# Kernel tuning notes

Measured on AMD Instinct MI355X. Metric: run time of the kernel, lower is better.

Reference implementation:

```python
import jax, jax.numpy as jnp
import numpy as np

N_NODES = 50000
N_EDGES = 800000
N_GRAPHS = 256
NEG_SLOPE = 0.2  # PyG GATConv default leaky_relu slope


def gat_conv(x, edge_index, W, a_src, a_dst, bias, concat):
    # x: [N, F_in], edge_index: [2, E] (row=source, col=dest), W: [F_in, H*C]
    N = x.shape[0]
    H, C = a_src.shape
    h = (x @ W).reshape(N, H, C)                       # [N, H, C]
    s_src = (h * a_src).sum(-1)                        # [N, H]
    s_dst = (h * a_dst).sum(-1)                        # [N, H]
    src, dst = edge_index[0], edge_index[1]
    alpha = jax.nn.leaky_relu(s_src[src] + s_dst[dst], NEG_SLOPE)  # [E, H]
    # softmax over edges grouped by destination node
    m = jax.ops.segment_max(alpha, dst, num_segments=N)
    alpha = jnp.exp(alpha - m[dst])
    denom = jax.ops.segment_sum(alpha, dst, num_segments=N)
    alpha = alpha / (denom[dst] + 1e-16)
    out = jax.ops.segment_sum(h[src] * alpha[:, :, None], dst, num_segments=N)  # [N, H, C]
    out = out.reshape(N, H * C) if concat else out.mean(axis=1)
    return out + bias


def setup_inputs() -> dict:
    key = jax.random.key(0)
    ks = jax.random.split(key, 12)
    x = jax.random.normal(ks[0], (N_NODES, 27), dtype=jnp.float32)
    edge_index = jax.random.randint(ks[1], (2, N_EDGES), 0, N_NODES, dtype=jnp.int64 if jax.config.jax_enable_x64 else jnp.int32)
    batch = (jnp.arange(N_NODES) * N_GRAPHS) // N_NODES  # sorted, every graph non-empty
    g = lambda k, shape, fan_in: jax.random.normal(k, shape, dtype=jnp.float32) * (1.0 / np.sqrt(fan_in))
    return {
        "x": x, "edge_index": edge_index, "batch": batch,
        "W1": g(ks[2], (27, 64), 27), "a_src1": g(ks[3], (4, 16), 16), "a_dst1": g(ks[4], (4, 16), 16), "b1": jnp.zeros((64,), jnp.float32),
        "W2": g(ks[5], (64, 256), 64), "a_src2": g(ks[6], (1, 256), 256), "a_dst2": g(ks[7], (1, 256), 256), "b2": jnp.zeros((256,), jnp.float32),
        "Wl1": g(ks[8], (256, 512), 256), "bl1": jnp.zeros((512,), jnp.float32),
        "Wl2": g(ks[9], (512, 1024), 512), "bl2": jnp.zeros((1024,), jnp.float32),
        "Wl3": g(ks[10], (1024, 4), 1024), "bl3": jnp.zeros((4,), jnp.float32),
    }


def reference(x, edge_index, batch, W1, a_src1, a_dst1, b1, W2, a_src2, a_dst2, b2, Wl1, bl1, Wl2, bl2, Wl3, bl3):
    N = x.shape[0]
    # add self loops (PyG GATConv default)
    loops = jnp.arange(N, dtype=edge_index.dtype)
    ei = jnp.concatenate([edge_index, jnp.stack([loops, loops])], axis=1)
    h = jax.nn.elu(gat_conv(x, ei, W1, a_src1, a_dst1, b1, concat=True))    # [N, 64]
    h = jax.nn.elu(gat_conv(h, ei, W2, a_src2, a_dst2, b2, concat=False))   # [N, 256]
    # global max pool per graph
    pooled = jax.ops.segment_max(h, batch, num_segments=N_GRAPHS)           # [G, 256]
    z = jax.nn.relu(pooled @ Wl1 + bl1)
    z = jax.nn.relu(z @ Wl2 + bl2)
    return z @ Wl3 + bl3                                                    # [G, 4] logits (CrossEntropyLoss branch)
```

## Files before the change

### kernel.cpp

```cpp
#include <hip/hip_runtime.h>
#include <hip/hip_fp16.h>
#include <math.h>

#define NEG_SLOPE 0.2f
#define SCANB 256
#define CAP 6144

__device__ __forceinline__ float leaky(float x) { return x >= 0.f ? x : NEG_SLOPE * x; }
__device__ __forceinline__ float elu(float x) { return x > 0.f ? x : expm1f(x); }

__device__ __forceinline__ unsigned encf(float f) {
    unsigned u = __float_as_uint(f);
    return (u & 0x80000000u) ? ~u : (u | 0x80000000u);
}

struct Half4 { __half2 a, b; };

typedef _Float16 half8 __attribute__((ext_vector_type(8)));
typedef float floatx4 __attribute__((ext_vector_type(4)));


__global__ __launch_bounds__(1024) void k_passA(const int* __restrict__ src,
                                                const int* __restrict__ dst, int E, int nbuck,
                                                int2* __restrict__ tmp, int* __restrict__ bcursor) {
    __shared__ int cnt[256];
    __shared__ int base[256];
    int t = threadIdx.x;
    if (t < 256) cnt[t] = 0;
    __syncthreads();
    int e0 = blockIdx.x * 4096;
    int s[4], d[4], r[4];
    bool v[4];
#pragma unroll
    for (int i = 0; i < 4; ++i) {
        int e = e0 + i * 1024 + t;
        v[i] = e < E;
        if (v[i]) {
            s[i] = src[e];
            d[i] = dst[e];
            r[i] = atomicAdd(&cnt[d[i] >> 8], 1);
        }
    }
    __syncthreads();
    if (t < nbuck) {
        int c = cnt[t];
        base[t] = c ? atomicAdd(&bcursor[t], c) : 0;
    }
    __syncthreads();
#pragma unroll
    for (int i = 0; i < 4; ++i) {
        if (v[i]) {
            int b = d[i] >> 8;
            int pos = base[b] + r[i];
            if (pos < CAP) tmp[(size_t)b * CAP + pos] = make_int2(s[i], d[i]);
        }
    }
}

__global__ __launch_bounds__(256) void k_B1s(const int2* __restrict__ tmp,
                                             const int* __restrict__ bcursor,
                                             int* __restrict__ offs, int* __restrict__ bsum,
                                             int N) {
    __shared__ int cnt[256];
    __shared__ int sm[256];
    int b = blockIdx.x, t = threadIdx.x;
    cnt[t] = 0;
    __syncthreads();
    int n = bcursor[b];
    if (n > CAP) n = CAP;
    for (int j = t; j < n; j += 256)
        atomicAdd(&cnt[tmp[(size_t)b * CAP + j].y & 255], 1);
    __syncthreads();
    int node = b * 256 + t;
    int v = (node < N) ? cnt[t] + 1 : 0;
    sm[t] = v;
    __syncthreads();
    for (int off = 1; off < 256; off <<= 1) {
        int u = (t >= off) ? sm[t - off] : 0;
        __syncthreads();
        sm[t] += u;
        __syncthreads();
    }
    if (node < N) offs[node] = sm[t] - v;
    if (t == 255) bsum[b] = sm[255];
}

__global__ void k_scan2(int* __restrict__ bsum, int nb) {
    __shared__ int sm[SCANB];
    int v = (threadIdx.x < nb) ? bsum[threadIdx.x] : 0;
    sm[threadIdx.x] = v;
    __syncthreads();
    for (int off = 1; off < SCANB; off <<= 1) {
        int t = (threadIdx.x >= off) ? sm[threadIdx.x - off] : 0;
        __syncthreads();
        sm[threadIdx.x] += t;
        __syncthreads();
    }
    if (threadIdx.x < nb) bsum[threadIdx.x] = sm[threadIdx.x] - v;
}

__global__ void k_scan3(int* __restrict__ offs, const int* __restrict__ bsum,
                        int* __restrict__ csr, int N, int EN) {
    int i = blockIdx.x * SCANB + threadIdx.x;
    if (i < N) {
        int v = offs[i] + bsum[blockIdx.x];
        offs[i] = v;
        csr[v] = i;
        if (i == N - 1) offs[N] = EN;
    }
}

__global__ __launch_bounds__(256) void k_B2(const int2* __restrict__ tmp,
                                            const int* __restrict__ bcursor,
                                            const int* __restrict__ offs,
                                            int* __restrict__ csr, int N) {
    __shared__ int cnt[256];
    int b = blockIdx.x, t = threadIdx.x;
    cnt[t] = 0;
    __syncthreads();
    int n = bcursor[b];
    if (n > CAP) n = CAP;
    for (int j = t; j < n; j += 256) {
        int2 sd = tmp[(size_t)b * CAP + j];
        int r = atomicAdd(&cnt[sd.y & 255], 1);
        csr[offs[sd.y] + 1 + r] = sd.x;
    }
}

__global__ void k_prep(const float* __restrict__ W2, __half* __restrict__ W2t,
                       const float* __restrict__ Wl1, __half* __restrict__ Wl1t,
                       const float* __restrict__ Wl2, __half* __restrict__ Wl2t,
                       const float* __restrict__ a_src2, const float* __restrict__ a_dst2,
                       float* __restrict__ ws2, float* __restrict__ wd2) {
    int i = blockIdx.x * blockDim.x + threadIdx.x;
    if (i < 16384) {
        int k = i >> 8, n = i & 255;
        W2t[(size_t)n * 64 + k] = __float2half(W2[i]);
    } else if (i < 16384 + 131072) {
        int j = i - 16384;
        int k = j >> 9, n = j & 511;
        Wl1t[(size_t)n * 256 + k] = __float2half(Wl1[j]);
    } else if (i < 16384 + 131072 + 524288) {
        int j = i - 16384 - 131072;
        int k = j >> 10, n = j & 1023;
        Wl2t[(size_t)n * 512 + k] = __float2half(Wl2[j]);
    } else if (i < 16384 + 131072 + 524288 + 128) {
        int j = i - 16384 - 131072 - 524288;
        int k = j & 63;
        const float* av = (j < 64) ? a_src2 : a_dst2;
        float acc = 0.f;
        for (int c = 0; c < 256; ++c) acc += W2[k * 256 + c] * av[c];
        if (j < 64) ws2[k] = acc; else wd2[k] = acc;
    }
}


__global__ void k_h1(const float* __restrict__ x, const float* __restrict__ W1,
                     const float* __restrict__ a_src, const float* __restrict__ a_dst,
                     __half* __restrict__ h1h, float* __restrict__ ssrc, float* __restrict__ sdst,
                     int N) {
    __shared__ float sW[27 * 64];
    for (int i = threadIdx.x; i < 27 * 64; i += blockDim.x) sW[i] = W1[i];
    __syncthreads();
    int wave = threadIdx.x >> 6;
    int lane = threadIdx.x & 63;
    int n = blockIdx.x * 4 + wave;
    if (n >= N) return;
    const float* xr = x + (size_t)n * 27;
    float acc = 0.f;
#pragma unroll
    for (int k = 0; k < 27; ++k) acc += xr[k] * sW[k * 64 + lane];
    h1h[(size_t)n * 64 + lane] = __float2half(acc);
    int hd = lane >> 4, c = lane & 15;
    float vs = acc * a_src[hd * 16 + c];
    float vd = acc * a_dst[hd * 16 + c];
#pragma unroll
    for (int off = 8; off >= 1; off >>= 1) {
        vs += __shfl_xor(vs, off);
        vd += __shfl_xor(vd, off);
    }
    if (c == 0) {
        ssrc[n * 4 + hd] = vs;
        sdst[n * 4 + hd] = vd;
    }
}

__global__ void k_msd1(const int* __restrict__ csr, const int* __restrict__ offs,
                       const float* __restrict__ ssrc, const float* __restrict__ sdst,
                       __half* __restrict__ e4h, float* __restrict__ dinv4, int N) {
    int i = blockIdx.x * blockDim.x + threadIdx.x;
    if (i >= N * 4) return;
    int n = i >> 2, hd = i & 3;
    int start = offs[n];
    int dg = offs[n + 1] - start;
    float sd = sdst[(size_t)n * 4 + hd];
    float den = 0.f;
    for (int j = 0; j < dg; ++j) {
        int s = csr[start + j];
        float e = expf(leaky(ssrc[(size_t)s * 4 + hd] + sd));
        den += e;
        e4h[(size_t)(start + j) * 4 + hd] = __float2half(e);
    }
    dinv4[(size_t)n * 4 + hd] = 1.f / (den + 1e-16f);
}

__global__ __launch_bounds__(64) void k_agg1(
        const int* __restrict__ csr, const int* __restrict__ offs,
        const __half* __restrict__ e4h, const float* __restrict__ dinv4,
        const __half* __restrict__ h1h, const float* __restrict__ bias,
        const float* __restrict__ ws2, const float* __restrict__ wd2,
        __half* __restrict__ out, float* __restrict__ ssrc2, float* __restrict__ sdst2, int N) {
    int d = blockIdx.x;
    int lane = threadIdx.x;
    int start = offs[d];
    int dg = offs[d + 1] - start;
    int hd = lane >> 4;
    float acc = 0.f;
#pragma unroll 4
    for (int j = 0; j < dg; ++j) {
        int s = csr[start + j];
        float w = __half2float(e4h[(size_t)(start + j) * 4 + hd]);
        acc += __half2float(h1h[(size_t)s * 64 + lane]) * w;
    }
    acc *= dinv4[(size_t)d * 4 + hd];
    float av = elu(acc + bias[lane]);
    out[(size_t)d * 64 + lane] = __float2half(av);
    float vs = av * ws2[lane];
    float vd = av * wd2[lane];
#pragma unroll
    for (int off = 32; off >= 1; off >>= 1) {
        vs += __shfl_xor(vs, off);
        vd += __shfl_xor(vd, off);
    }
    if (lane == 0) { ssrc2[d] = vs; sdst2[d] = vd; }
}


__global__ void k_msd2(const int* __restrict__ csr, const int* __restrict__ offs,
                       const float* __restrict__ ssrc, const float* __restrict__ sdst,
                       __half* __restrict__ e1h, float* __restrict__ dinv1, int N) {
    int n = blockIdx.x * blockDim.x + threadIdx.x;
    if (n >= N) return;
    int start = offs[n];
    int dg = offs[n + 1] - start;
    float sd = sdst[n];
    float den = 0.f;
#pragma unroll 2
    for (int j = 0; j < dg; ++j) {
        float e = expf(leaky(ssrc[csr[start + j]] + sd));
        den += e;
        e1h[start + j] = __float2half(e);
    }
    dinv1[n] = 1.f / (den + 1e-16f);
}

__global__ __launch_bounds__(64) void k_agg2(
        const int* __restrict__ csr, const int* __restrict__ offs,
        const __half* __restrict__ e1h, const float* __restrict__ dinv1,
        const __half* __restrict__ act1h, __half* __restrict__ aggh, int N) {
    int d = blockIdx.x;
    int lane = threadIdx.x;
    int start = offs[d];
    int dg = offs[d + 1] - start;
    float acc = 0.f;
#pragma unroll 4
    for (int j = 0; j < dg; ++j) {
        int s = csr[start + j];
        float w = __half2float(e1h[start + j]);
        acc += __half2float(act1h[(size_t)s * 64 + lane]) * w;
    }
    acc *= dinv1[d];
    aggh[(size_t)d * 64 + lane] = __float2half(acc);
}

__global__ void k_h2b(const __half* __restrict__ aggh, const __half* __restrict__ W2t,
                      const float* __restrict__ b2, const int* __restrict__ batch,
                      unsigned* __restrict__ pooledU, int N) {
    int t = threadIdx.x;
    int wv = t >> 6, lane = t & 63;
    int lr = lane & 15, lg = lane >> 4;
    int n0 = blockIdx.x * 16;

    half8 a0 = {0, 0, 0, 0, 0, 0, 0, 0};
    half8 a1 = {0, 0, 0, 0, 0, 0, 0, 0};
    int nodeA = n0 + lr;
    if (nodeA < N) {
        a0 = *(const half8*)(aggh + (size_t)nodeA * 64 + lg * 8);
        a1 = *(const half8*)(aggh + (size_t)nodeA * 64 + 32 + lg * 8);
    }
    int gFirst = batch[n0];
    int gLast  = batch[min(n0 + 15, N - 1)];
    bool uni = (gFirst == gLast);
#pragma unroll
    for (int c = 0; c < 4; ++c) {
        int col = wv * 64 + c * 16 + lr;
        half8 b0 = *(const half8*)(W2t + (size_t)col * 64 + lg * 8);
        half8 b1 = *(const half8*)(W2t + (size_t)col * 64 + 32 + lg * 8);
        floatx4 acc = {0.f, 0.f, 0.f, 0.f};
        acc = __builtin_amdgcn_mfma_f32_16x16x32_f16(a0, b0, acc, 0, 0, 0);
        acc = __builtin_amdgcn_mfma_f32_16x16x32_f16(a1, b1, acc, 0, 0, 0);
        float bv = b2[col];
        float v0 = elu(acc[0] + bv);
        float v1 = elu(acc[1] + bv);
        float v2 = elu(acc[2] + bv);
        float v3 = elu(acc[3] + bv);
        if (uni) {
            float vm = fmaxf(fmaxf(v0, v1), fmaxf(v2, v3));
            vm = fmaxf(vm, __shfl_xor(vm, 16));
            vm = fmaxf(vm, __shfl_xor(vm, 32));
            if (lg == 0) atomicMax(&pooledU[gFirst * 256 + col], encf(vm));
        } else {
            float vr[4] = {v0, v1, v2, v3};
#pragma unroll
            for (int r = 0; r < 4; ++r) {
                int node = n0 + lg * 4 + r;
                if (node < N) atomicMax(&pooledU[batch[node] * 256 + col], encf(vr[r]));
            }
        }
    }
}

__global__ void k_dec(const unsigned* __restrict__ pooledU, __half* __restrict__ pooledh) {
    int i = blockIdx.x * 256 + threadIdx.x;
    unsigned u = pooledU[i];
    u = (u & 0x80000000u) ? (u & 0x7FFFFFFFu) : ~u;
    pooledh[i] = __float2half(__uint_as_float(u));
}


__global__ void k_gemm(const __half* __restrict__ A, const __half* __restrict__ Wt,
                       const float* __restrict__ bias, __half* __restrict__ C,
                       int M, int N, int K, int relu) {
    int t = threadIdx.x;
    int wv = t >> 6, lane = t & 63;
    int lr = lane & 15, lg = lane >> 4;
    int bx = blockIdx.x, by = blockIdx.y;
    int arow = by * 64 + wv * 16 + lr;
    floatx4 acc[4] = {{0.f,0.f,0.f,0.f},{0.f,0.f,0.f,0.f},{0.f,0.f,0.f,0.f},{0.f,0.f,0.f,0.f}};
    for (int k0 = 0; k0 < K; k0 += 32) {
        half8 a = *(const half8*)(A + (size_t)arow * K + k0 + lg * 8);
#pragma unroll
        for (int c = 0; c < 4; ++c) {
            int col = bx * 64 + c * 16 + lr;
            half8 b = *(const half8*)(Wt + (size_t)col * K + k0 + lg * 8);
            acc[c] = __builtin_amdgcn_mfma_f32_16x16x32_f16(a, b, acc[c], 0, 0, 0);
        }
    }
#pragma unroll
    for (int c = 0; c < 4; ++c) {
        int col = bx * 64 + c * 16 + lr;
        float bv = bias[col];
#pragma unroll
        for (int r = 0; r < 4; ++r) {
            int row = by * 64 + wv * 16 + lg * 4 + r;
            float v = acc[c][r] + bv;
            if (relu) v = fmaxf(v, 0.f);
            C[(size_t)row * N + col] = __float2half(v);
        }
    }
}

__global__ void k_mlp3(const __half* __restrict__ z2, const float* __restrict__ Wl3,
                       const float* __restrict__ bl3, float* __restrict__ out, int G) {
    __shared__ float sT[16];
    int g = blockIdx.x, t = threadIdx.x;
    int wave = t >> 6, lane = t & 63;
    float p[4] = {0.f, 0.f, 0.f, 0.f};
#pragma unroll
    for (int kk = 0; kk < 4; ++kk) {
        int k = t + kk * 256;
        float z = __half2float(z2[(size_t)g * 1024 + k]);
        float4 w = ((const float4*)Wl3)[k];
        p[0] += z * w.x; p[1] += z * w.y; p[2] += z * w.z; p[3] += z * w.w;
    }
#pragma unroll
    for (int c = 0; c < 4; ++c) {
#pragma unroll
        for (int off = 32; off >= 1; off >>= 1) p[c] += __shfl_xor(p[c], off);
        if (lane == 0) sT[wave * 4 + c] = p[c];
    }
    __syncthreads();
    if (t < 4) {
        float v = bl3[t] + sT[t] + sT[4 + t] + sT[8 + t] + sT[12 + t];
        out[(size_t)g * 4 + t] = v;
    }
}

extern "C" void kernel_launch(void* const* d_in, const int* in_sizes, int n_in,
                              void* d_out, int out_size, void* d_ws, size_t ws_size,
                              hipStream_t stream) {
    const float* x      = (const float*)d_in[0];
    const int*   ei     = (const int*)d_in[1];
    const int*   batch  = (const int*)d_in[2];
    const float* W1     = (const float*)d_in[3];
    const float* a_src1 = (const float*)d_in[4];
    const float* a_dst1 = (const float*)d_in[5];
    const float* b1     = (const float*)d_in[6];
    const float* W2     = (const float*)d_in[7];
    const float* a_src2 = (const float*)d_in[8];
    const float* a_dst2 = (const float*)d_in[9];
    const float* b2     = (const float*)d_in[10];
    const float* Wl1    = (const float*)d_in[11];
    const float* bl1    = (const float*)d_in[12];
    const float* Wl2    = (const float*)d_in[13];
    const float* bl2    = (const float*)d_in[14];
    const float* Wl3    = (const float*)d_in[15];
    const float* bl3    = (const float*)d_in[16];

    const int N = in_sizes[0] / 27;
    const int E = in_sizes[1] / 2;
    const int G = out_size / 4;
    const int EN = E + N;
    const int nbuck = (N + 255) >> 8;

    const int* srcA = ei;
    const int* dstA = ei + E;

    char* wp = (char*)d_ws;
    auto take = [&](size_t bytes) { char* p = wp; wp += (bytes + 15) & ~(size_t)15; return p; };

    int2* tmp     = (int2*)take((size_t)256 * CAP * 8);
    int* bcursor  = (int*)take(256 * 4);
    int* offs     = (int*)take((size_t)(N + 1) * 4);
    int* bsum     = (int*)take((size_t)SCANB * 4);
    int* csr      = (int*)take((size_t)EN * 4);

    float* ssrc1  = (float*)take((size_t)N * 4 * 4);
    float* sdst1  = (float*)take((size_t)N * 4 * 4);
    float* ssrc2  = (float*)take((size_t)N * 4);
    float* sdst2  = (float*)take((size_t)N * 4);
    float* dinv4  = (float*)take((size_t)N * 4 * 4);
    float* dinv1  = (float*)take((size_t)N * 4);
    float* ws2    = (float*)take(64 * 4);
    float* wd2    = (float*)take(64 * 4);
    unsigned* pooledU = (unsigned*)take((size_t)G * 256 * 4);

    __half* h1h   = (__half*)take((size_t)N * 64 * 2);
    __half* act1h = (__half*)take((size_t)N * 64 * 2);
    __half* aggh  = (__half*)take((size_t)N * 64 * 2);
    __half* e4h   = (__half*)take((size_t)EN * 4 * 2);
    __half* e1h   = (__half*)take((size_t)EN * 2);
    __half* W2t   = (__half*)take((size_t)64 * 256 * 2);
    __half* Wl1t  = (__half*)take((size_t)512 * 256 * 2);
    __half* Wl2t  = (__half*)take((size_t)1024 * 512 * 2);
    __half* pooledh = (__half*)take((size_t)G * 256 * 2);
    __half* z1h   = (__half*)take((size_t)G * 512 * 2);
    __half* z2h   = (__half*)take((size_t)G * 1024 * 2);

    const int nb = (N + SCANB - 1) / SCANB;

    {
        int tot = 16384 + 131072 + 524288 + 128;
        k_prep<<<(tot + 255) / 256, 256, 0, stream>>>(W2, W2t, Wl1, Wl1t, Wl2, Wl2t,
                                                      a_src2, a_dst2, ws2, wd2);
    }

    hipMemsetAsync(bcursor, 0, 256 * 4, stream);
    hipMemsetAsync(pooledU, 0, (size_t)G * 256 * 4, stream);
    k_passA<<<(E + 4095) / 4096, 1024, 0, stream>>>(srcA, dstA, E, nbuck, tmp, bcursor);
    k_B1s<<<nbuck, 256, 0, stream>>>(tmp, bcursor, offs, bsum, N);
    k_scan2<<<1, SCANB, 0, stream>>>(bsum, nb);
    k_scan3<<<nb, SCANB, 0, stream>>>(offs, bsum, csr, N, EN);
    k_B2<<<nbuck, 256, 0, stream>>>(tmp, bcursor, offs, csr, N);

    k_h1<<<(N + 3) / 4, 256, 0, stream>>>(x, W1, a_src1, a_dst1, h1h, ssrc1, sdst1, N);
    k_msd1<<<(N * 4 + 255) / 256, 256, 0, stream>>>(csr, offs, ssrc1, sdst1, e4h, dinv4, N);
    k_agg1<<<N, 64, 0, stream>>>(csr, offs, e4h, dinv4, h1h, b1, ws2, wd2,
                                 act1h, ssrc2, sdst2, N);

    k_msd2<<<(N + 255) / 256, 256, 0, stream>>>(csr, offs, ssrc2, sdst2, e1h, dinv1, N);
    k_agg2<<<N, 64, 0, stream>>>(csr, offs, e1h, dinv1, act1h, aggh, N);
    k_h2b<<<(N + 15) / 16, 256, 0, stream>>>(aggh, W2t, b2, batch, pooledU, N);

    k_dec<<<G, 256, 0, stream>>>(pooledU, pooledh);
    k_gemm<<<dim3(512 / 64, 256 / 64), 256, 0, stream>>>(pooledh, Wl1t, bl1, z1h, 256, 512, 256, 1);
    k_gemm<<<dim3(1024 / 64, 256 / 64), 256, 0, stream>>>(z1h, Wl2t, bl2, z2h, 256, 1024, 512, 1);
    k_mlp3<<<G, 256, 0, stream>>>(z2h, Wl3, bl3, (float*)d_out, G);
}
```

Before: 207.7 us.

## Fuse preprocessing, CSR build and MLP tail kernels to cut launch count

Merges the bucket pass with the weight prep into one launch, and folds the three CSR scan kernels into a single kernel that uses a decoupled lookback over per-block aggregates. The pooled-decode step moves into the first MLP GEMM, and the final linear layer is fused into the second GEMM via atomic adds into a bias-initialised output. The two memsets become one init kernel. This removes about seven launches and some intermediate buffers. The cost is spin-waiting between blocks, which assumes all scan blocks are co-resident, and non-deterministic float atomics on the output.

```diff
diff --git a/kernel.cpp b/kernel.cpp
--- a/kernel.cpp
+++ b/kernel.cpp
@@ -3,7 +3,6 @@
 #include <math.h>
 
 #define NEG_SLOPE 0.2f
-#define SCANB 256
 #define CAP 6144
 
 __device__ __forceinline__ float leaky(float x) { return x >= 0.f ? x : NEG_SLOPE * x; }
@@ -13,63 +12,109 @@
     unsigned u = __float_as_uint(f);
     return (u & 0x80000000u) ? ~u : (u | 0x80000000u);
 }
-
-struct Half4 { __half2 a, b; };
+__device__ __forceinline__ float decf(unsigned u) {
+    u = (u & 0x80000000u) ? (u & 0x7FFFFFFFu) : ~u;
+    return __uint_as_float(u);
+}
 
 typedef _Float16 half8 __attribute__((ext_vector_type(8)));
 typedef float floatx4 __attribute__((ext_vector_type(4)));
 
-
-__global__ __launch_bounds__(1024) void k_passA(const int* __restrict__ src,
-                                                const int* __restrict__ dst, int E, int nbuck,
-                                                int2* __restrict__ tmp, int* __restrict__ bcursor) {
-    __shared__ int cnt[256];
-    __shared__ int base[256];
+__global__ void k_init(int* __restrict__ bcursor, int* __restrict__ aggP,
+                       unsigned* __restrict__ pooledU, float* __restrict__ out,
+                       const float* __restrict__ bl3, int G) {
+    int i = blockIdx.x * 256 + threadIdx.x;
+    if (i < 256) bcursor[i] = 0;
+    else if (i < 512) aggP[i - 256] = 0;
+    else if (i < 512 + G * 256) pooledU[i - 512] = 0u;
+    else if (i < 512 + G * 256 + G * 4) {
+        int j = i - 512 - G * 256;
+        out[j] = bl3[j & 3];
+    }
+}
+
+__global__ __launch_bounds__(1024) void k_pp(const int* __restrict__ src,
+                                             const int* __restrict__ dst, int E, int nbuck,
+                                             int2* __restrict__ tmp, int* __restrict__ bcursor,
+                                             const float* __restrict__ W2, __half* __restrict__ W2t,
+                                             const float* __restrict__ Wl1, __half* __restrict__ Wl1t,
+                                             const float* __restrict__ Wl2, __half* __restrict__ Wl2t,
+                                             const float* __restrict__ a_src2,
+                                             const float* __restrict__ a_dst2,
+                                             float* __restrict__ ws2, float* __restrict__ wd2,
+                                             int nA) {
     int t = threadIdx.x;
-    if (t < 256) cnt[t] = 0;
-    __syncthreads();
-    int e0 = blockIdx.x * 4096;
-    int s[4], d[4], r[4];
-    bool v[4];
-#pragma unroll
-    for (int i = 0; i < 4; ++i) {
-        int e = e0 + i * 1024 + t;
-        v[i] = e < E;
-        if (v[i]) {
-            s[i] = src[e];
-            d[i] = dst[e];
-            r[i] = atomicAdd(&cnt[d[i] >> 8], 1);
-        }
-    }
-    __syncthreads();
-    if (t < nbuck) {
-        int c = cnt[t];
-        base[t] = c ? atomicAdd(&bcursor[t], c) : 0;
-    }
-    __syncthreads();
-#pragma unroll
-    for (int i = 0; i < 4; ++i) {
-        if (v[i]) {
-            int b = d[i] >> 8;
-            int pos = base[b] + r[i];
-            if (pos < CAP) tmp[(size_t)b * CAP + pos] = make_int2(s[i], d[i]);
-        }
-    }
-}
-
-__global__ __launch_bounds__(256) void k_B1s(const int2* __restrict__ tmp,
+    if ((int)blockIdx.x < nA) {
+        __shared__ int cnt[256];
+        __shared__ int base[256];
+        if (t < 256) cnt[t] = 0;
+        __syncthreads();
+        int e0 = blockIdx.x * 4096;
+        int s[4], d[4], r[4];
+        bool v[4];
+#pragma unroll
+        for (int i = 0; i < 4; ++i) {
+            int e = e0 + i * 1024 + t;
+            v[i] = e < E;
+            if (v[i]) {
+                s[i] = src[e];
+                d[i] = dst[e];
+                r[i] = atomicAdd(&cnt[d[i] >> 8], 1);
+            }
+        }
+        __syncthreads();
+        if (t < nbuck) {
+            int c = cnt[t];
+            base[t] = c ? atomicAdd(&bcursor[t], c) : 0;
+        }
+        __syncthreads();
+#pragma unroll
+        for (int i = 0; i < 4; ++i) {
+            if (v[i]) {
+                int b = d[i] >> 8;
+                int pos = base[b] + r[i];
+                if (pos < CAP) tmp[(size_t)b * CAP + pos] = make_int2(s[i], d[i]);
+            }
+        }
+    } else {
+        int i = (blockIdx.x - nA) * 1024 + t;
+        if (i < 16384) {
+            int k = i >> 8, n = i & 255;
+            W2t[(size_t)n * 64 + k] = __float2half(W2[i]);
+        } else if (i < 16384 + 131072) {
+            int j = i - 16384;
+            int k = j >> 9, n = j & 511;
+            Wl1t[(size_t)n * 256 + k] = __float2half(Wl1[j]);
+        } else if (i < 16384 + 131072 + 524288) {
+            int j = i - 16384 - 131072;
+            int k = j >> 10, n = j & 1023;
+            Wl2t[(size_t)n * 512 + k] = __float2half(Wl2[j]);
+        } else if (i < 16384 + 131072 + 524288 + 128) {
+            int j = i - 16384 - 131072 - 524288;
+            int k = j & 63;
+            const float* av = (j < 64) ? a_src2 : a_dst2;
+            float acc = 0.f;
+            for (int c = 0; c < 256; ++c) acc += W2[k * 256 + c] * av[c];
+            if (j < 64) ws2[k] = acc; else wd2[k] = acc;
+        }
+    }
+}
+
+__global__ __launch_bounds__(256) void k_csr(const int2* __restrict__ tmp,
                                              const int* __restrict__ bcursor,
-                                             int* __restrict__ offs, int* __restrict__ bsum,
-                                             int N) {
+                                             int* __restrict__ aggP, int* __restrict__ offs,
+                                             int* __restrict__ csr, int N, int EN) {
     __shared__ int cnt[256];
     __shared__ int sm[256];
+    __shared__ int red[256];
+    __shared__ int foffs[256];
     int b = blockIdx.x, t = threadIdx.x;
     cnt[t] = 0;
     __syncthreads();
     int n = bcursor[b];
     if (n > CAP) n = CAP;
-    for (int j = t; j < n; j += 256)
-        atomicAdd(&cnt[tmp[(size_t)b * CAP + j].y & 255], 1);
+    const int2* tb = tmp + (size_t)b * CAP;
+    for (int j = t; j < n; j += 256) atomicAdd(&cnt[tb[j].y & 255], 1);
     __syncthreads();
     int node = b * 256 + t;
     int v = (node < N) ? cnt[t] + 1 : 0;
@@ -81,76 +126,36 @@
         sm[t] += u;
         __syncthreads();
     }
-    if (node < N) offs[node] = sm[t] - v;
-    if (t == 255) bsum[b] = sm[255];
-}
-
-__global__ void k_scan2(int* __restrict__ bsum, int nb) {
-    __shared__ int sm[SCANB];
-    int v = (threadIdx.x < nb) ? bsum[threadIdx.x] : 0;
-    sm[threadIdx.x] = v;
+    if (t == 0) {
+        __threadfence();
+        atomicExch(&aggP[b], sm[255]);
+    }
+    int part = 0;
+    if (t < b) {
+        int val;
+        while ((val = atomicAdd(&aggP[t], 0)) == 0) __builtin_amdgcn_s_sleep(2);
+        part = val;
+    }
+    red[t] = part;
     __syncthreads();
-    for (int off = 1; off < SCANB; off <<= 1) {
-        int t = (threadIdx.x >= off) ? sm[threadIdx.x - off] : 0;
+    for (int off = 128; off >= 1; off >>= 1) {
+        if (t < off) red[t] += red[t + off];
         __syncthreads();
-        sm[threadIdx.x] += t;
-        __syncthreads();
-    }
-    if (threadIdx.x < nb) bsum[threadIdx.x] = sm[threadIdx.x] - v;
-}
-
-__global__ void k_scan3(int* __restrict__ offs, const int* __restrict__ bsum,
-                        int* __restrict__ csr, int N, int EN) {
-    int i = blockIdx.x * SCANB + threadIdx.x;
-    if (i < N) {
-        int v = offs[i] + bsum[blockIdx.x];
-        offs[i] = v;
-        csr[v] = i;
-        if (i == N - 1) offs[N] = EN;
-    }
-}
-
-__global__ __launch_bounds__(256) void k_B2(const int2* __restrict__ tmp,
-                                            const int* __restrict__ bcursor,
-                                            const int* __restrict__ offs,
-                                            int* __restrict__ csr, int N) {
-    __shared__ int cnt[256];
-    int b = blockIdx.x, t = threadIdx.x;
+    }
+    int myoff = red[0] + sm[t] - v;
+    foffs[t] = myoff;
+    if (node < N) {
+        offs[node] = myoff;
+        csr[myoff] = node;
+        if (node == N - 1) offs[N] = EN;
+    }
     cnt[t] = 0;
     __syncthreads();
-    int n = bcursor[b];
-    if (n > CAP) n = CAP;
     for (int j = t; j < n; j += 256) {
-        int2 sd = tmp[(size_t)b * CAP + j];
-        int r = atomicAdd(&cnt[sd.y & 255], 1);
-        csr[offs[sd.y] + 1 + r] = sd.x;
-    }
-}
-
-__global__ void k_prep(const float* __restrict__ W2, __half* __restrict__ W2t,
-                       const float* __restrict__ Wl1, __half* __restrict__ Wl1t,
-                       const float* __restrict__ Wl2, __half* __restrict__ Wl2t,
-                       const float* __restrict__ a_src2, const float* __restrict__ a_dst2,
-                       float* __restrict__ ws2, float* __restrict__ wd2) {
-    int i = blockIdx.x * blockDim.x + threadIdx.x;
-    if (i < 16384) {
-        int k = i >> 8, n = i & 255;
-        W2t[(size_t)n * 64 + k] = __float2half(W2[i]);
-    } else if (i < 16384 + 131072) {
-        int j = i - 16384;
-        int k = j >> 9, n = j & 511;
-        Wl1t[(size_t)n * 256 + k] = __float2half(Wl1[j]);
-    } else if (i < 16384 + 131072 + 524288) {
-        int j = i - 16384 - 131072;
-        int k = j >> 10, n = j & 1023;
-        Wl2t[(size_t)n * 512 + k] = __float2half(Wl2[j]);
-    } else if (i < 16384 + 131072 + 524288 + 128) {
-        int j = i - 16384 - 131072 - 524288;
-        int k = j & 63;
-        const float* av = (j < 64) ? a_src2 : a_dst2;
-        float acc = 0.f;
-        for (int c = 0; c < 256; ++c) acc += W2[k * 256 + c] * av[c];
-        if (j < 64) ws2[k] = acc; else wd2[k] = acc;
+        int2 sd = tb[j];
+        int li = sd.y & 255;
+        int r = atomicAdd(&cnt[li], 1);
+        csr[foffs[li] + 1 + r] = sd.x;
     }
 }
 
@@ -320,29 +325,28 @@
     }
 }
 
-__global__ void k_dec(const unsigned* __restrict__ pooledU, __half* __restrict__ pooledh) {
-    int i = blockIdx.x * 256 + threadIdx.x;
-    unsigned u = pooledU[i];
-    u = (u & 0x80000000u) ? (u & 0x7FFFFFFFu) : ~u;
-    pooledh[i] = __float2half(__uint_as_float(u));
-}
-
-
-__global__ void k_gemm(const __half* __restrict__ A, const __half* __restrict__ Wt,
-                       const float* __restrict__ bias, __half* __restrict__ C,
-                       int M, int N, int K, int relu) {
+
+__global__ void k_gemm1d(const unsigned* __restrict__ pooledU, const __half* __restrict__ Wt,
+                         const float* __restrict__ bias, __half* __restrict__ C) {
     int t = threadIdx.x;
     int wv = t >> 6, lane = t & 63;
     int lr = lane & 15, lg = lane >> 4;
     int bx = blockIdx.x, by = blockIdx.y;
     int arow = by * 64 + wv * 16 + lr;
     floatx4 acc[4] = {{0.f,0.f,0.f,0.f},{0.f,0.f,0.f,0.f},{0.f,0.f,0.f,0.f},{0.f,0.f,0.f,0.f}};
-    for (int k0 = 0; k0 < K; k0 += 32) {
-        half8 a = *(const half8*)(A + (size_t)arow * K + k0 + lg * 8);
+    for (int k0 = 0; k0 < 256; k0 += 32) {
+        const unsigned* pu = pooledU + (size_t)arow * 256 + k0 + lg * 8;
+        uint4 u0 = *(const uint4*)pu;
+        uint4 u1 = *(const uint4*)(pu + 4);
+        half8 a;
+        a[0] = (_Float16)decf(u0.x); a[1] = (_Float16)decf(u0.y);
+        a[2] = (_Float16)decf(u0.z); a[3] = (_Float16)decf(u0.w);
+        a[4] = (_Float16)decf(u1.x); a[5] = (_Float16)decf(u1.y);
+        a[6] = (_Float16)decf(u1.z); a[7] = (_Float16)decf(u1.w);
 #pragma unroll
         for (int c = 0; c < 4; ++c) {
             int col = bx * 64 + c * 16 + lr;
-            half8 b = *(const half8*)(Wt + (size_t)col * K + k0 + lg * 8);
+            half8 b = *(const half8*)(Wt + (size_t)col * 256 + k0 + lg * 8);
             acc[c] = __builtin_amdgcn_mfma_f32_16x16x32_f16(a, b, acc[c], 0, 0, 0);
         }
     }
@@ -353,36 +357,57 @@
 #pragma unroll
         for (int r = 0; r < 4; ++r) {
             int row = by * 64 + wv * 16 + lg * 4 + r;
-            float v = acc[c][r] + bv;
-            if (relu) v = fmaxf(v, 0.f);
-            C[(size_t)row * N + col] = __float2half(v);
-        }
-    }
-}
-
-__global__ void k_mlp3(const __half* __restrict__ z2, const float* __restrict__ Wl3,
-                       const float* __restrict__ bl3, float* __restrict__ out, int G) {
-    __shared__ float sT[16];
-    int g = blockIdx.x, t = threadIdx.x;
-    int wave = t >> 6, lane = t & 63;
-    float p[4] = {0.f, 0.f, 0.f, 0.f};
-#pragma unroll
-    for (int kk = 0; kk < 4; ++kk) {
-        int k = t + kk * 256;
-        float z = __half2float(z2[(size_t)g * 1024 + k]);
-        float4 w = ((const float4*)Wl3)[k];
-        p[0] += z * w.x; p[1] += z * w.y; p[2] += z * w.z; p[3] += z * w.w;
-    }
+            C[(size_t)row * 512 + col] = __float2half(fmaxf(acc[c][r] + bv, 0.f));
+        }
+    }
+}
+
+__global__ void k_gemm2h(const __half* __restrict__ A, const __half* __restrict__ Wt,
+                         const float* __restrict__ bias, const float* __restrict__ Wl3,
+                         float* __restrict__ out) {
+    int t = threadIdx.x;
+    int wv = t >> 6, lane = t & 63;
+    int lr = lane & 15, lg = lane >> 4;
+    int bx = blockIdx.x, by = blockIdx.y;
+    int arow = by * 64 + wv * 16 + lr;
+    floatx4 acc[4] = {{0.f,0.f,0.f,0.f},{0.f,0.f,0.f,0.f},{0.f,0.f,0.f,0.f},{0.f,0.f,0.f,0.f}};
+    for (int k0 = 0; k0 < 512; k0 += 32) {
+        half8 a = *(const half8*)(A + (size_t)arow * 512 + k0 + lg * 8);
+#pragma unroll
+        for (int c = 0; c < 4; ++c) {
+            int col = bx * 64 + c * 16 + lr;
+            half8 b = *(const half8*)(Wt + (size_t)col * 512 + k0 + lg * 8);
+            acc[c] = __builtin_amdgcn_mfma_f32_16x16x32_f16(a, b, acc[c], 0, 0, 0);
+        }
+    }
+    float p[4][4] = {{0.f}};
 #pragma unroll
     for (int c = 0; c < 4; ++c) {
-#pragma unroll
-        for (int off = 32; off >= 1; off >>= 1) p[c] += __shfl_xor(p[c], off);
-        if (lane == 0) sT[wave * 4 + c] = p[c];
-    }
-    __syncthreads();
-    if (t < 4) {
-        float v = bl3[t] + sT[t] + sT[4 + t] + sT[8 + t] + sT[12 + t];
-        out[(size_t)g * 4 + t] = v;
+        int col = bx * 64 + c * 16 + lr;
+        float bv = bias[col];
+        float4 w3 = ((const float4*)Wl3)[col];
+#pragma unroll
+        for (int r = 0; r < 4; ++r) {
+            float z = fmaxf(acc[c][r] + bv, 0.f);
+            p[r][0] += z * w3.x;
+            p[r][1] += z * w3.y;
+            p[r][2] += z * w3.z;
+            p[r][3] += z * w3.w;
+        }
+    }
+#pragma unroll
+    for (int off = 8; off >= 1; off >>= 1)
+#pragma unroll
+        for (int r = 0; r < 4; ++r)
+#pragma unroll
+            for (int k4 = 0; k4 < 4; ++k4) p[r][k4] += __shfl_xor(p[r][k4], off);
+    if (lr == 0) {
+#pragma unroll
+        for (int r = 0; r < 4; ++r) {
+            int row = by * 64 + wv * 16 + lg * 4 + r;
+#pragma unroll
+            for (int k4 = 0; k4 < 4; ++k4) atomicAdd(&out[row * 4 + k4], p[r][k4]);
+        }
     }
 }
 
@@ -421,8 +446,8 @@
 
     int2* tmp     = (int2*)take((size_t)256 * CAP * 8);
     int* bcursor  = (int*)take(256 * 4);
+    int* aggP     = (int*)take(256 * 4);
     int* offs     = (int*)take((size_t)(N + 1) * 4);
-    int* bsum     = (int*)take((size_t)SCANB * 4);
     int* csr      = (int*)take((size_t)EN * 4);
 
     float* ssrc1  = (float*)take((size_t)N * 4 * 4);
@@ -443,25 +468,24 @@
     __half* W2t   = (__half*)take((size_t)64 * 256 * 2);
     __half* Wl1t  = (__half*)take((size_t)512 * 256 * 2);
     __half* Wl2t  = (__half*)take((size_t)1024 * 512 * 2);
-    __half* pooledh = (__half*)take((size_t)G * 256 * 2);
     __half* z1h   = (__half*)take((size_t)G * 512 * 2);
-    __half* z2h   = (__half*)take((size_t)G * 1024 * 2);
-
-    const int nb = (N + SCANB - 1) / SCANB;
 
     {
-        int tot = 16384 + 131072 + 524288 + 128;
-        k_prep<<<(tot + 255) / 256, 256, 0, stream>>>(W2, W2t, Wl1, Wl1t, Wl2, Wl2t,
-                                                      a_src2, a_dst2, ws2, wd2);
-    }
-
-    hipMemsetAsync(bcursor, 0, 256 * 4, stream);
-    hipMemsetAsync(pooledU, 0, (size_t)G * 256 * 4, stream);
-    k_passA<<<(E + 4095) / 4096, 1024, 0, stream>>>(srcA, dstA, E, nbuck, tmp, bcursor);
-    k_B1s<<<nbuck, 256, 0, stream>>>(tmp, bcursor, offs, bsum, N);
-    k_scan2<<<1, SCANB, 0, stream>>>(bsum, nb);
-    k_scan3<<<nb, SCANB, 0, stream>>>(offs, bsum, csr, N, EN);
-    k_B2<<<nbuck, 256, 0, stream>>>(tmp, bcursor, offs, csr, N);
+        int tot = 512 + G * 256 + G * 4;
+        k_init<<<(tot + 255) / 256, 256, 0, stream>>>(bcursor, aggP, pooledU,
+                                                      (float*)d_out, bl3, G);
+    }
+
+    {
+        const int nA = (E + 4095) / 4096;
+        const int prepTot = 16384 + 131072 + 524288 + 128;
+        const int nP = (prepTot + 1023) / 1024;
+        k_pp<<<nA + nP, 1024, 0, stream>>>(srcA, dstA, E, nbuck, tmp, bcursor,
+                                           W2, W2t, Wl1, Wl1t, Wl2, Wl2t,
+                                           a_src2, a_dst2, ws2, wd2, nA);
+    }
+
+    k_csr<<<nbuck, 256, 0, stream>>>(tmp, bcursor, aggP, offs, csr, N, EN);
 
     k_h1<<<(N + 3) / 4, 256, 0, stream>>>(x, W1, a_src1, a_dst1, h1h, ssrc1, sdst1, N);
     k_msd1<<<(N * 4 + 255) / 256, 256, 0, stream>>>(csr, offs, ssrc1, sdst1, e4h, dinv4, N);
@@ -472,8 +496,6 @@
     k_agg2<<<N, 64, 0, stream>>>(csr, offs, e1h, dinv1, act1h, aggh, N);
     k_h2b<<<(N + 15) / 16, 256, 0, stream>>>(aggh, W2t, b2, batch, pooledU, N);
 
-    k_dec<<<G, 256, 0, stream>>>(pooledU, pooledh);
-    k_gemm<<<dim3(512 / 64, 256 / 64), 256, 0, stream>>>(pooledh, Wl1t, bl1, z1h, 256, 512, 256, 1);
-    k_gemm<<<dim3(1024 / 64, 256 / 64), 256, 0, stream>>>(z1h, Wl2t, bl2, z2h, 256, 1024, 512, 1);
-    k_mlp3<<<G, 256, 0, stream>>>(z2h, Wl3, bl3, (float*)d_out, G);
-}
+    k_gemm1d<<<dim3(8, 4), 256, 0, stream>>>(pooledU, Wl1t, bl1, z1h);
+    k_gemm2h<<<dim3(16, 4), 256, 0, stream>>>(z1h, Wl2t, bl2, Wl3, (float*)d_out);
+}
```

Result: no change. 209.1 us (+0.7%).
